# Kernel optimization log

Hardware: AMD Instinct MI355X
Metric: run time of the kernel (lower is better)

## Reference

```python
import jax, jax.numpy as jnp
import numpy as np

B, LQ, D, DFF, NH, DH, NL, NP = 8, 1024, 256, 1024, 8, 32, 3, 4
_SHAPES = np.array([[100, 100], [50, 50], [25, 25]], dtype=np.int32)  # (H, W) per level
_AREAS = _SHAPES[:, 0] * _SHAPES[:, 1]
LIN = int(_AREAS.sum())  # 13125
_STARTS = np.concatenate([[0], np.cumsum(_AREAS)[:-1]]).astype(np.int32)


def setup_inputs() -> dict:
    key = jax.random.key(0)
    ks = iter(jax.random.split(key, 64))
    def rn(shape, s=1.0):
        return jax.random.normal(next(ks), shape, jnp.float32) * s
    return {
        "query_embed": rn((B, LQ, D)),
        "query_mask": jnp.zeros((B, LQ), bool),  # True = padded key
        "query_order": rn((B, LQ, D)),
        "values": rn((B, LIN, D)),
        "ref_point": jax.random.uniform(next(ks), (B, LQ, 2), jnp.float32),
        "ref_pos": rn((B, LQ, D)),
        "ref_feat": rn((B, LQ, D)),
        "shapes": jnp.asarray(_SHAPES),
        "level_start": jnp.asarray(_STARTS),
        "headwise_refpoint_idxs": jnp.zeros((B, LQ), jnp.int32),  # unused (side_head=0)
        # self-attention sub-block params (nn.MultiheadAttention packed in-proj)
        "sa_in_w": rn((D, 3 * D), 0.02), "sa_in_b": jnp.zeros((3 * D,)),
        "sa_out_w": rn((D, D), 0.02), "sa_out_b": jnp.zeros((D,)),
        "sa_ln1_g": jnp.ones((D,)), "sa_ln1_b": jnp.zeros((D,)),
        "sa_l1_w": rn((D, DFF), 0.02), "sa_l1_b": jnp.zeros((DFF,)),
        "sa_l2_w": rn((DFF, D), 0.02), "sa_l2_b": jnp.zeros((D,)),
        "sa_ln2_g": jnp.ones((D,)), "sa_ln2_b": jnp.zeros((D,)),
        # MDeformAttn params
        "da_val_w": rn((D, D), 0.02), "da_val_b": jnp.zeros((D,)),
        "da_off_w": rn((D, NH * NL * NP * 2), 0.001), "da_off_b": rn((NH * NL * NP * 2,), 0.01),
        "da_att_w": rn((D, NH * NL * NP), 0.02), "da_att_b": jnp.zeros((NH * NL * NP,)),
        "da_out_w": rn((D, D), 0.02), "da_out_b": jnp.zeros((D,)),
        # post-deform FFN block params
        "ln1_g": jnp.ones((D,)), "ln1_b": jnp.zeros((D,)),
        "ff1_w": rn((D, DFF), 0.02), "ff1_b": jnp.zeros((DFF,)),
        "ff2_w": rn((DFF, D), 0.02), "ff2_b": jnp.zeros((D,)),
        "ln2_g": jnp.ones((D,)), "ln2_b": jnp.zeros((D,)),
    }


def _ln(x, g, b):
    m = jnp.mean(x, -1, keepdims=True)
    v = jnp.mean((x - m) ** 2, -1, keepdims=True)
    return (x - m) / jnp.sqrt(v + 1e-5) * g + b


def _mha(q, k, v, key_padding_mask, in_w, in_b, out_w, out_b):
    Bv = q.shape[0]
    qp = (q @ in_w[:, :D] + in_b[:D]).reshape(Bv, -1, NH, DH)
    kp = (k @ in_w[:, D:2 * D] + in_b[D:2 * D]).reshape(Bv, -1, NH, DH)
    vp = (v @ in_w[:, 2 * D:] + in_b[2 * D:]).reshape(Bv, -1, NH, DH)
    scores = jnp.einsum('bqhd,bkhd->bhqk', qp, kp) / jnp.sqrt(jnp.float32(DH))
    scores = scores + jnp.where(key_padding_mask[:, None, None, :], -1e9, 0.0)
    a = jax.nn.softmax(scores, -1)
    o = jnp.einsum('bhqk,bkhd->bqhd', a, vp).reshape(Bv, -1, D)
    return o @ out_w + out_b


def _ms_deform(query, ref_point, values, shapes,
               val_w, val_b, off_w, off_b, att_w, att_b, out_w, out_b):
    # Multi-scale deformable attention (MDeformAttn, align_corners=False bilinear, zero pad)
    Bv, Lq = query.shape[0], query.shape[1]
    v = (values @ val_w + val_b).reshape(Bv, -1, NH, DH)
    off = (query @ off_w + off_b).reshape(Bv, Lq, NH, NL, NP, 2)
    attn = jax.nn.softmax((query @ att_w + att_b).reshape(Bv, Lq, NH, NL * NP), -1)
    attn = attn.reshape(Bv, Lq, NH, NL, NP)
    norm = jnp.stack([shapes[:, 1], shapes[:, 0]], -1).astype(jnp.float32)  # (W, H)
    loc = ref_point[:, :, None, None, None, :] + off / norm[None, None, None, :, None, :]
    acc = 0.0
    for lvl in range(NL):  # static spatial shapes per level
        Hl, Wl = int(_SHAPES[lvl, 0]), int(_SHAPES[lvl, 1])
        s = int(_STARTS[lvl])
        vl = v[:, s:s + Hl * Wl].transpose(0, 2, 1, 3)  # [B,NH,Hl*Wl,DH]
        ll = loc[:, :, :, lvl]                          # [B,Lq,NH,NP,2]
        x = ll[..., 0] * Wl - 0.5
        y = ll[..., 1] * Hl - 0.5
        x0 = jnp.floor(x); y0 = jnp.floor(y)
        wx = x - x0; wy = y - y0
        x0i = x0.astype(jnp.int32); y0i = y0.astype(jnp.int32)
        def tw(w):  # [B,Lq,NH,NP] -> [B,NH,Lq*NP,1]
            return w.transpose(0, 2, 1, 3).reshape(Bv, NH, -1, 1)
        def gather(yy, xx):
            valid = ((yy >= 0) & (yy < Hl) & (xx >= 0) & (xx < Wl))
            idx = jnp.clip(yy, 0, Hl - 1) * Wl + jnp.clip(xx, 0, Wl - 1)
            idx_t = idx.transpose(0, 2, 1, 3).reshape(Bv, NH, -1)
            g = jnp.take_along_axis(vl, idx_t[..., None], axis=2)  # [B,NH,Lq*NP,DH]
            return g * tw(valid.astype(vl.dtype))
        samp = (tw((1 - wy) * (1 - wx)) * gather(y0i, x0i)
                + tw((1 - wy) * wx) * gather(y0i, x0i + 1)
                + tw(wy * (1 - wx)) * gather(y0i + 1, x0i)
                + tw(wy * wx) * gather(y0i + 1, x0i + 1))
        aw = tw(attn[:, :, :, lvl])
        acc = acc + (samp * aw).reshape(Bv, NH, Lq, NP, DH).sum(3)
    out = acc.transpose(0, 2, 1, 3).reshape(Bv, Lq, D)
    return out @ out_w + out_b


def reference(query_embed, query_mask, query_order, values, ref_point, ref_pos, ref_feat,
              shapes, level_start, headwise_refpoint_idxs,
              sa_in_w, sa_in_b, sa_out_w, sa_out_b, sa_ln1_g, sa_ln1_b,
              sa_l1_w, sa_l1_b, sa_l2_w, sa_l2_b, sa_ln2_g, sa_ln2_b,
              da_val_w, da_val_b, da_off_w, da_off_b, da_att_w, da_att_b, da_out_w, da_out_b,
              ln1_g, ln1_b, ff1_w, ff1_b, ff2_w, ff2_b, ln2_g, ln2_b):
    # forward_self_att(tgt + ref_feat, query_order + ref_pos, query_mask); dropout = identity (eval)
    src = query_embed + ref_feat
    pos = query_order + ref_pos
    q = src + pos
    src = _ln(src + _mha(q, q, src, query_mask, sa_in_w, sa_in_b, sa_out_w, sa_out_b), sa_ln1_g, sa_ln1_b)
    src = _ln(src + (jax.nn.relu(src @ sa_l1_w + sa_l1_b) @ sa_l2_w + sa_l2_b), sa_ln2_g, sa_ln2_b)
    tgt = src
    dq = tgt + query_order + ref_pos + ref_feat
    tgt2 = _ms_deform(dq, ref_point, values, shapes,
                      da_val_w, da_val_b, da_off_w, da_off_b, da_att_w, da_att_b, da_out_w, da_out_b)
    tgt = _ln(tgt + tgt2, ln1_g, ln1_b)
    tgt = _ln(tgt + (jax.nn.relu(tgt @ ff1_w + ff1_b) @ ff2_w + ff2_b), ln2_g, ln2_b)
    return tgt
```

## Files before the change

kernel.cpp:

```cpp
#include <hip/hip_runtime.h>
#include <math.h>

#define B_   8
#define LQ_  1024
#define D_   256
#define NH_  8
#define DH_  32
#define LIN_ 13125

typedef __attribute__((ext_vector_type(4))) float f32x4;
typedef __attribute__((ext_vector_type(8))) short bf16x8;
typedef __attribute__((ext_vector_type(4))) short bf16x4;

__device__ __forceinline__ float4 f4add(float4 a, float4 b){
  return make_float4(a.x+b.x, a.y+b.y, a.z+b.z, a.w+b.w);
}
__device__ __forceinline__ unsigned short f2bf(float f){
  unsigned u = __float_as_uint(f);
  unsigned r = (u + 0x7fffu + ((u>>16)&1u)) >> 16;
  return (unsigned short)r;
}
__device__ __forceinline__ float bf2f(unsigned short u){
  return __uint_as_float(((unsigned)u)<<16);
}
__device__ __forceinline__ unsigned pk2(float a, float b){
  return (unsigned)f2bf(a) | ((unsigned)f2bf(b)<<16);
}
__device__ __forceinline__ float fexp2(float x){
#if __has_builtin(__builtin_amdgcn_exp2f)
  return __builtin_amdgcn_exp2f(x);
#else
  return exp2f(x);
#endif
}
__device__ __forceinline__ f32x4 mfma16x16(bf16x4 a, bf16x4 b, f32x4 c){
#if __has_builtin(__builtin_amdgcn_mfma_f32_16x16x16_bf16)
  return __builtin_amdgcn_mfma_f32_16x16x16_bf16(a, b, c, 0, 0, 0);
#else
  asm volatile("s_nop 1\n\tv_mfma_f32_16x16x16_bf16 %0, %1, %2, %0"
               : "+v"(c) : "v"(a), "v"(b));
  return c;
#endif
}
__device__ __forceinline__ void gload16(const void* g, void* l){
  __builtin_amdgcn_global_load_lds(
      (const __attribute__((address_space(1))) void*)g,
      (__attribute__((address_space(3))) void*)l, 16, 0, 0);
}
__device__ __forceinline__ int xcd_swz(int lin, int nwg){
  if (nwg < 64) return lin;
  const int q = nwg >> 3, r = nwg & 7;
  const int x = lin & 7, d = lin >> 3;
  return (x < r ? x*(q+1) : r*(q+1) + (x-r)*q) + d;
}

__global__ __launch_bounds__(256) void k_prep(
    const float4* __restrict__ qe, const float4* __restrict__ rf,
    const float4* __restrict__ qo, const float4* __restrict__ rp,
    const unsigned char* __restrict__ mask,
    const float* __restrict__ off_b, const float* __restrict__ att_b,
    float4* __restrict__ src, uint2* __restrict__ srcb, uint2* __restrict__ qb,
    float* __restrict__ biasf, float* __restrict__ biasoa)
{
  int i = blockIdx.x*256 + threadIdx.x;
  if (i < B_*LQ_) biasf[i] = mask[i] ? -2.0e9f : 0.f;
  if (blockIdx.x == 32) {
    for (int j = threadIdx.x; j < 384; j += 256)
      biasoa[j] = (j < 192) ? off_b[j] : (j < 288 ? att_b[j-192] : 0.f);
  }
  float4 s = f4add(qe[i], rf[i]);
  src[i] = s;
  float4 q = f4add(s, f4add(qo[i], rp[i]));
  srcb[i] = make_uint2(pk2(s.x,s.y), pk2(s.z,s.w));
  qb[i]   = make_uint2(pk2(q.x,q.y), pk2(q.z,q.w));
}

struct WEnt { const float* s; unsigned short* d; int K; int N; };
struct WPack { WEnt e[10]; };
__global__ __launch_bounds__(256) void k_wtcvt(WPack p)
{
  __shared__ float sm[32][33];
  WEnt w = p.e[blockIdx.y];
  const int tk = w.K >> 5, tn = w.N >> 5;
  const int nt = tk * tn;
  const int r = threadIdx.x >> 5, c = threadIdx.x & 31;
  for (int tile = blockIdx.x; tile < nt; tile += gridDim.x) {
    const int ti = tile / tn, tj = tile % tn;
    #pragma unroll
    for (int rr = r; rr < 32; rr += 8)
      sm[rr][c] = w.s[(size_t)(ti*32+rr)*w.N + tj*32 + c];
    __syncthreads();
    #pragma unroll
    for (int rr = r; rr < 32; rr += 8)
      w.d[(size_t)(tj*32+rr)*w.K + ti*32 + c] = f2bf(sm[c][rr]);
    __syncthreads();
  }
}

__global__ __launch_bounds__(256) void k_f2b8(
    const float4* __restrict__ in, uint4* __restrict__ out)
{
  const int i = blockIdx.x*256 + threadIdx.x;
  float4 a = in[2*i], b = in[2*i+1];
  out[i] = make_uint4(pk2(a.x,a.y), pk2(a.z,a.w), pk2(b.x,b.y), pk2(b.z,b.w));
}

template<bool BF16OUT>
__global__ __launch_bounds__(256) void k_gemm_bf(
    const unsigned short* __restrict__ A, int lda,
    const unsigned short* __restrict__ Wt,
    const float* __restrict__ bias,
    float* __restrict__ Cf, unsigned short* __restrict__ Cb, int ldc,
    int M, int N, int K, int relu)
{
  __shared__ unsigned short As[2][4096];
  __shared__ unsigned short Bs[2][4096];
  const int t = threadIdx.x;
  const int lin = xcd_swz(blockIdx.y*gridDim.x + blockIdx.x, gridDim.x*gridDim.y);
  const int bx = lin % gridDim.x, by = lin / gridDim.x;
  const int m0 = by * 128;
  const int n0 = bx * 128;
  const int w  = t >> 6, lane = t & 63;
  const int lr = lane & 15, lg = lane >> 4;
  const int wm = (w & 1) * 64, wn = (w >> 1) * 64;

  const int rowc  = t >> 2;
  const int cbs8  = (((t & 3) ^ ((t >> 2) & 3)) << 3);
  const size_t ra0 = (size_t)min(m0 + rowc,      M-1) * lda;
  const size_t ra1 = (size_t)min(m0 + rowc + 64, M-1) * lda;
  const size_t rb0 = (size_t)(n0 + rowc)      * K;
  const size_t rb1 = (size_t)(n0 + rowc + 64) * K;
  unsigned short* la0[2] = { &As[0][(w<<9)],        &As[1][(w<<9)] };
  unsigned short* la1[2] = { &As[0][2048+(w<<9)],   &As[1][2048+(w<<9)] };
  unsigned short* lb0[2] = { &Bs[0][(w<<9)],        &Bs[1][(w<<9)] };
  unsigned short* lb1[2] = { &Bs[0][2048+(w<<9)],   &Bs[1][2048+(w<<9)] };

  f32x4 acc[4][4];
  #pragma unroll
  for (int i=0;i<4;++i)
    #pragma unroll
    for (int j=0;j<4;++j) acc[i][j] = (f32x4){0.f,0.f,0.f,0.f};

  const int cswz = ((lg ^ (lr & 3)) << 3);
  const int nt = K >> 5;

  {
    gload16(A  + ra0 + cbs8, la0[0]);
    gload16(A  + ra1 + cbs8, la1[0]);
    gload16(Wt + rb0 + cbs8, lb0[0]);
    gload16(Wt + rb1 + cbs8, lb1[0]);
  }
  for (int ks = 0; ks < nt; ++ks) {
    const int cur = ks & 1;
    __syncthreads();
    if (ks + 1 < nt) {
      const int kb = (ks + 1) << 5;
      const int nb = cur ^ 1;
      gload16(A  + ra0 + kb + cbs8, la0[nb]);
      gload16(A  + ra1 + kb + cbs8, la1[nb]);
      gload16(Wt + rb0 + kb + cbs8, lb0[nb]);
      gload16(Wt + rb1 + kb + cbs8, lb1[nb]);
    }
    bf16x8 af[4], bfr[4];
    #pragma unroll
    for (int mi=0;mi<4;++mi)
      af[mi]  = *reinterpret_cast<const bf16x8*>(&As[cur][(wm+mi*16+lr)*32 + cswz]);
    #pragma unroll
    for (int ni=0;ni<4;++ni)
      bfr[ni] = *reinterpret_cast<const bf16x8*>(&Bs[cur][(wn+ni*16+lr)*32 + cswz]);
    #pragma unroll
    for (int mi=0;mi<4;++mi)
      #pragma unroll
      for (int ni=0;ni<4;++ni)
        acc[mi][ni] = __builtin_amdgcn_mfma_f32_16x16x32_bf16(af[mi], bfr[ni], acc[mi][ni], 0, 0, 0);
  }

  float bs[4];
  #pragma unroll
  for (int ni=0;ni<4;++ni) bs[ni] = bias[n0 + wn + ni*16 + lr];
  #pragma unroll
  for (int mi=0;mi<4;++mi){
    #pragma unroll
    for (int i=0;i<4;++i){
      const int row = m0 + wm + mi*16 + lg*4 + i;
      if (row >= M) continue;
      #pragma unroll
      for (int ni=0;ni<4;++ni){
        const int col = n0 + wn + ni*16 + lr;
        float v = acc[mi][ni][i] + bs[ni];
        if (relu) v = fmaxf(v, 0.f);
        if (BF16OUT) Cb[(size_t)row*ldc + col] = f2bf(v);
        else         Cf[(size_t)row*ldc + col] = v;
      }
    }
  }
}

template<int EPI>
__global__ __launch_bounds__(256) void k_gemm64(
    const unsigned short* __restrict__ A, int lda,
    const unsigned short* __restrict__ Wt,
    const float* __restrict__ bias,
    float* __restrict__ Cf, unsigned short* __restrict__ Cb, int ldc,
    int M, int N, int K, int relu)
{
  __shared__ unsigned short As[2][4096];
  __shared__ unsigned short Bs[2][4096];
  const int t = threadIdx.x;
  const int lin = xcd_swz(blockIdx.y*gridDim.x + blockIdx.x, gridDim.x*gridDim.y);
  const int bx = lin % gridDim.x, by = lin / gridDim.x;
  const int m0 = by * 64;
  const int n0 = bx * 64;
  const int w = t >> 6, lane = t & 63;
  const int lr = lane & 15, lg = lane >> 4;
  const int wm = (w & 1) * 32, wn = (w >> 1) * 32;

  const int c0 = w*64 + lane;
  const int c1 = 256 + w*64 + lane;
  const int r0c = c0 >> 3, s0c = ((c0 & 7) ^ (r0c & 7)) << 3;
  const int r1c = c1 >> 3, s1c = ((c1 & 7) ^ (r1c & 7)) << 3;
  const size_t a0 = (size_t)(m0 + r0c)*lda + s0c;
  const size_t a1 = (size_t)(m0 + r1c)*lda + s1c;
  const size_t b0 = (size_t)(n0 + r0c)*K + s0c;
  const size_t b1 = (size_t)(n0 + r1c)*K + s1c;
  const int d0 = w*512, d1 = 2048 + w*512;

  f32x4 acc[2][2];
  acc[0][0]=acc[0][1]=acc[1][0]=acc[1][1]=(f32x4){0.f,0.f,0.f,0.f};

  gload16(A + a0, &As[0][d0]);  gload16(A + a1, &As[0][d1]);
  gload16(Wt + b0, &Bs[0][d0]); gload16(Wt + b1, &Bs[0][d1]);
  const int nt = K >> 6;
  for (int ks = 0; ks < nt; ++ks) {
    const int cur = ks & 1;
    __syncthreads();
    if (ks + 1 < nt) {
      const int kb = (ks + 1) << 6;
      const int nb = cur ^ 1;
      gload16(A + kb + a0, &As[nb][d0]);  gload16(A + kb + a1, &As[nb][d1]);
      gload16(Wt + kb + b0, &Bs[nb][d0]); gload16(Wt + kb + b1, &Bs[nb][d1]);
    }
    bf16x8 af[2][2], bfr[2][2];
    #pragma unroll
    for (int mi=0;mi<2;++mi){
      const int r = wm + mi*16 + lr;
      #pragma unroll
      for (int kk=0;kk<2;++kk){
        const int ch = ((kk*4 + lg) ^ (r & 7)) << 3;
        af[mi][kk] = *reinterpret_cast<const bf16x8*>(&As[cur][r*64 + ch]);
      }
    }
    #pragma unroll
    for (int ni=0;ni<2;++ni){
      const int r = wn + ni*16 + lr;
      #pragma unroll
      for (int kk=0;kk<2;++kk){
        const int ch = ((kk*4 + lg) ^ (r & 7)) << 3;
        bfr[ni][kk] = *reinterpret_cast<const bf16x8*>(&Bs[cur][r*64 + ch]);
      }
    }
    #pragma unroll
    for (int kk=0;kk<2;++kk)
      #pragma unroll
      for (int mi=0;mi<2;++mi)
        #pragma unroll
        for (int ni=0;ni<2;++ni)
          acc[mi][ni] = __builtin_amdgcn_mfma_f32_16x16x32_bf16(af[mi][kk], bfr[ni][kk], acc[mi][ni], 0, 0, 0);
  }

  float bs[2];
  bs[0] = bias[n0 + wn + lr];
  bs[1] = bias[n0 + wn + 16 + lr];
  if (EPI == 3) {
    #pragma unroll
    for (int mi=0;mi<2;++mi){
      const int rowb = m0 + wm + mi*16 + lg*4;
      #pragma unroll
      for (int ni=0;ni<2;++ni){
        const int colb = n0 + wn + ni*16 + lr;
        const int bh = (rowb >> 10)*8 + (colb >> 5);
        const int d = colb & 31;
        ushort4 pkv;
        pkv.x = f2bf(acc[mi][ni][0] + bs[ni]);
        pkv.y = f2bf(acc[mi][ni][1] + bs[ni]);
        pkv.z = f2bf(acc[mi][ni][2] + bs[ni]);
        pkv.w = f2bf(acc[mi][ni][3] + bs[ni]);
        *reinterpret_cast<ushort4*>(Cb + (size_t)bh*32768 + (size_t)d*1024 + (rowb & 1023)) = pkv;
      }
    }
    return;
  }
  #pragma unroll
  for (int mi=0;mi<2;++mi){
    #pragma unroll
    for (int i=0;i<4;++i){
      const int row = m0 + wm + mi*16 + lg*4 + i;
      #pragma unroll
      for (int ni=0;ni<2;++ni){
        const int col = n0 + wn + ni*16 + lr;
        float v = acc[mi][ni][i] + bs[ni];
        if (relu) v = fmaxf(v, 0.f);
        if (EPI == 0) {
          Cf[(size_t)row*ldc + col] = v;
        } else if (EPI == 1) {
          Cb[(size_t)row*ldc + col] = f2bf(v);
        } else {
          const int ch = col & 255;
          const int sel = col >> 8;
          const int bh = (row >> 10)*8 + (ch >> 5);
          Cb[(size_t)sel*2097152 + (size_t)bh*32768 + (size_t)(row & 1023)*32 + (ch & 31)] = f2bf(v);
        }
      }
    }
  }
}

__global__ __launch_bounds__(256) void k_gemm_ln(
    const unsigned short* __restrict__ A, int lda,
    const unsigned short* __restrict__ Wt,
    const float* __restrict__ bias,
    const float* __restrict__ X,
    const float* __restrict__ g, const float* __restrict__ be,
    float* __restrict__ out,
    unsigned short* __restrict__ ab,
    const float* __restrict__ qo, const float* __restrict__ rp,
    const float* __restrict__ rf, unsigned short* __restrict__ dqb,
    int K)
{
  __shared__ unsigned short As[2][1024];
  __shared__ unsigned short Bs[2][16384];
  __shared__ float part[4][16][2];
  const int t = threadIdx.x;
  const int w = t >> 6, lane = t & 63;
  const int lr = lane & 15, lg = lane >> 4;
  const int m0 = xcd_swz(blockIdx.x, gridDim.x) * 16;

  const int ar = t >> 3, ac = t & 7;
  const size_t aSrc = (size_t)(m0 + ar)*lda + ((ac ^ (ar & 7)) << 3);
  size_t bSrc[8];
  #pragma unroll
  for (int q=0;q<8;++q){
    const int c = q*256 + t;
    const int br = c >> 3, bc = c & 7;
    bSrc[q] = (size_t)br*K + ((bc ^ (br & 7)) << 3);
  }

  f32x4 acc[4];
  #pragma unroll
  for (int ni=0;ni<4;++ni) acc[ni] = (f32x4){0.f,0.f,0.f,0.f};

  if (w < 2) gload16(A + aSrc, &As[0][(w<<9)]);
  #pragma unroll
  for (int q=0;q<8;++q) gload16(Wt + bSrc[q], &Bs[0][q*2048 + (w<<9)]);

  const int nt = K >> 6;
  for (int ks = 0; ks < nt; ++ks) {
    const int cur = ks & 1;
    __syncthreads();
    if (ks + 1 < nt) {
      const int kb = (ks + 1) << 6;
      const int nb = cur ^ 1;
      if (w < 2) gload16(A + kb + aSrc, &As[nb][(w<<9)]);
      #pragma unroll
      for (int q=0;q<8;++q) gload16(Wt + kb + bSrc[q], &Bs[nb][q*2048 + (w<<9)]);
    }
    bf16x8 af[2];
    #pragma unroll
    for (int kk=0;kk<2;++kk){
      const int ch = ((kk*4 + lg) ^ (lr & 7)) << 3;
      af[kk] = *reinterpret_cast<const bf16x8*>(&As[cur][lr*64 + ch]);
    }
    #pragma unroll
    for (int ni=0;ni<4;++ni){
      const int r = w*64 + ni*16 + lr;
      #pragma unroll
      for (int kk=0;kk<2;++kk){
        const int ch = ((kk*4 + lg) ^ (r & 7)) << 3;
        bf16x8 bfv = *reinterpret_cast<const bf16x8*>(&Bs[cur][r*64 + ch]);
        acc[ni] = __builtin_amdgcn_mfma_f32_16x16x32_bf16(af[kk], bfv, acc[ni], 0, 0, 0);
      }
    }
  }

  float v[4][4];
  int colv[4];
  #pragma unroll
  for (int ni=0;ni<4;++ni) colv[ni] = w*64 + ni*16 + lr;
  #pragma unroll
  for (int ni=0;ni<4;++ni){
    const float bsv = bias[colv[ni]];
    #pragma unroll
    for (int i=0;i<4;++i){
      const int row = m0 + lg*4 + i;
      v[ni][i] = acc[ni][i] + bsv + X[(size_t)row*256 + colv[ni]];
    }
  }
  #pragma unroll
  for (int i=0;i<4;++i){
    float s1 = v[0][i]+v[1][i]+v[2][i]+v[3][i];
    float s2 = v[0][i]*v[0][i]+v[1][i]*v[1][i]+v[2][i]*v[2][i]+v[3][i]*v[3][i];
    #pragma unroll
    for (int o=1;o<16;o<<=1){ s1 += __shfl_xor(s1,o,64); s2 += __shfl_xor(s2,o,64); }
    if (lr == 0){ part[w][lg*4+i][0] = s1; part[w][lg*4+i][1] = s2; }
  }
  __syncthreads();
  #pragma unroll
  for (int i=0;i<4;++i){
    const int rl = lg*4 + i;
    const float S1 = part[0][rl][0]+part[1][rl][0]+part[2][rl][0]+part[3][rl][0];
    const float S2 = part[0][rl][1]+part[1][rl][1]+part[2][rl][1]+part[3][rl][1];
    const float mean = S1 * 0.00390625f;
    const float var  = S2 * 0.00390625f - mean*mean;
    const float rstd = rsqrtf(var + 1e-5f);
    const size_t row = m0 + rl;
    #pragma unroll
    for (int ni=0;ni<4;++ni){
      const int col = colv[ni];
      const float o = (v[ni][i]-mean)*rstd*g[col] + be[col];
      out[row*256 + col] = o;
      if (ab) ab[row*256 + col] = f2bf(o);
      if (dqb) {
        const float e = qo[row*256+col] + rp[row*256+col] + rf[row*256+col];
        dqb[row*256 + col] = f2bf(o + e);
      }
    }
  }
}

__global__ __launch_bounds__(256) void k_attn2(
    const unsigned short* __restrict__ Qbf,
    const unsigned short* __restrict__ Kbf,
    const unsigned short* __restrict__ Vtb,
    const float* __restrict__ biasf,
    unsigned short* __restrict__ Ob)
{
  __shared__ unsigned short Klds[2][2048];
  __shared__ unsigned short Vlds[2][2048];
  __shared__ float Blds[1024];
  const int t = threadIdx.x;
  const int wv = t >> 6, lane = t & 63;
  const int lin = xcd_swz(blockIdx.y*gridDim.x + blockIdx.x, gridDim.x*gridDim.y);
  const int bx = lin % gridDim.x, by = lin / gridDim.x;
  const int qt = bx * 4 + wv;
  const int bh = by;
  const int b = bh >> 3;
  const int q0 = qt << 4;
  const int lr = lane & 15, lg = lane >> 4;

  bf16x8 qf = *reinterpret_cast<const bf16x8*>(
      Qbf + (size_t)bh*32768 + (size_t)(q0 + lr)*32 + lg*8);

  *reinterpret_cast<float4*>(&Blds[t*4]) =
      *reinterpret_cast<const float4*>(biasf + b*1024 + t*4);

  const unsigned short* Kg = Kbf + (size_t)bh*32768;
  const unsigned short* Vg = Vtb + (size_t)bh*32768;

  const int kRow   = lane >> 2;
  const int kChunk = (lane & 3) ^ (kRow & 3);
  const size_t kSrc = (size_t)(wv*16 + kRow)*32 + (kChunk<<3);
  const int vDim   = lane >> 3;
  const int vChunk = (lane & 7) ^ vDim;
  const size_t vSrc = (size_t)(wv*8 + vDim)*1024 + (vChunk<<3);
  unsigned short* kDst[2] = { &Klds[0][wv<<9], &Klds[1][wv<<9] };
  unsigned short* vDst[2] = { &Vlds[0][wv<<9], &Vlds[1][wv<<9] };

  gload16(Kg + kSrc, kDst[0]);
  gload16(Vg + vSrc, vDst[0]);
  __syncthreads();

  f32x4 acc0 = {0.f,0.f,0.f,0.f}, acc1 = {0.f,0.f,0.f,0.f};
  float m_run = -1e30f, l_run = 0.f;
  const float Cs = 0.17677669529663687f * 1.4426950408889634f;
  const int kswz = (lg ^ (lr & 3)) << 3;

  for (int kt = 0; kt < 16; ++kt) {
    const int cur = kt & 1;
    if (kt + 1 < 16) {
      const size_t k0n = (size_t)(kt + 1) << 6;
      gload16(Kg + k0n*32 + kSrc, kDst[cur^1]);
      gload16(Vg + k0n    + vSrc, vDst[cur^1]);
    }
    f32x4 st[4];
    __builtin_amdgcn_s_setprio(1);
    #pragma unroll
    for (int j=0;j<4;++j){
      bf16x8 kf = *reinterpret_cast<const bf16x8*>(&Klds[cur][(16*j + lr)*32 + kswz]);
      f32x4 z = {0.f,0.f,0.f,0.f};
      st[j] = __builtin_amdgcn_mfma_f32_16x16x32_bf16(kf, qf, z, 0, 0, 0);
    }
    __builtin_amdgcn_s_setprio(0);
    const int k0 = kt << 6;
    float s[16];
    #pragma unroll
    for (int j=0;j<4;++j){
      float4 bv = *reinterpret_cast<const float4*>(&Blds[k0 + 16*j + lg*4]);
      s[4*j+0] = fmaf(st[j][0], Cs, bv.x);
      s[4*j+1] = fmaf(st[j][1], Cs, bv.y);
      s[4*j+2] = fmaf(st[j][2], Cs, bv.z);
      s[4*j+3] = fmaf(st[j][3], Cs, bv.w);
    }
    float mc = fmaxf(fmaxf(fmaxf(s[0],s[1]),fmaxf(s[2],s[3])),
                     fmaxf(fmaxf(s[4],s[5]),fmaxf(s[6],s[7])));
    float mc2 = fmaxf(fmaxf(fmaxf(s[8],s[9]),fmaxf(s[10],s[11])),
                      fmaxf(fmaxf(s[12],s[13]),fmaxf(s[14],s[15])));
    mc = fmaxf(mc, mc2);
    mc = fmaxf(mc, __shfl_xor(mc, 16, 64));
    mc = fmaxf(mc, __shfl_xor(mc, 32, 64));
    if (!__all(mc <= m_run + 8.f)) {
      float m_new = fmaxf(m_run, mc);
      float sc = fexp2(m_run - m_new);
      l_run *= sc;
      m_run = m_new;
      float sc0 = __shfl(sc, lg*4+0, 64);
      float sc1 = __shfl(sc, lg*4+1, 64);
      float sc2 = __shfl(sc, lg*4+2, 64);
      float sc3 = __shfl(sc, lg*4+3, 64);
      acc0[0]*=sc0; acc0[1]*=sc1; acc0[2]*=sc2; acc0[3]*=sc3;
      acc1[0]*=sc0; acc1[1]*=sc1; acc1[2]*=sc2; acc1[3]*=sc3;
    }
    float p[16];
    #pragma unroll
    for (int i=0;i<16;++i) p[i] = fexp2(s[i] - m_run);
    float ps = 0.f;
    #pragma unroll
    for (int i=0;i<16;++i) ps += p[i];
    ps += __shfl_xor(ps, 16, 64);
    ps += __shfl_xor(ps, 32, 64);
    l_run += ps;
    bf16x4 pb[4];
    #pragma unroll
    for (int j=0;j<4;++j){
      unsigned lo, hi;
      asm("v_cvt_pk_bf16_f32 %0, %1, %2" : "=v"(lo) : "v"(p[4*j+0]), "v"(p[4*j+1]));
      asm("v_cvt_pk_bf16_f32 %0, %1, %2" : "=v"(hi) : "v"(p[4*j+2]), "v"(p[4*j+3]));
      uint2 u = make_uint2(lo, hi);
      pb[j] = __builtin_bit_cast(bf16x4, u);
    }
    __builtin_amdgcn_s_setprio(1);
    #pragma unroll
    for (int j=0;j<4;++j){
      const int coff = (((2*j + (lg>>1)) ^ (lr & 7)) << 3) + ((lg & 1) << 2);
      bf16x4 v0 = *reinterpret_cast<const bf16x4*>(&Vlds[cur][lr*64 + coff]);
      bf16x4 v1 = *reinterpret_cast<const bf16x4*>(&Vlds[cur][(16+lr)*64 + coff]);
      acc0 = mfma16x16(pb[j], v0, acc0);
      acc1 = mfma16x16(pb[j], v1, acc1);
    }
    __builtin_amdgcn_s_setprio(0);
    __syncthreads();
  }
  float li[4];
  #pragma unroll
  for (int i=0;i<4;++i) li[i] = 1.f / __shfl(l_run, lg*4+i, 64);
  const int h = bh & 7;
  unsigned short* orow = Ob + (size_t)(b*1024 + q0)*256 + h*32;
  #pragma unroll
  for (int i=0;i<4;++i){
    orow[(size_t)(lg*4+i)*256 + lr]      = f2bf(acc0[i]*li[i]);
    orow[(size_t)(lg*4+i)*256 + 16 + lr] = f2bf(acc1[i]*li[i]);
  }
}

__global__ __launch_bounds__(256) void k_dgather2(
    const unsigned short* __restrict__ vproj,
    const float* __restrict__ IJ,
    const float* __restrict__ refp,
    unsigned short* __restrict__ outb)
{
  __shared__ int   ilds[8][12][4];
  __shared__ float wlds[8][12][4];
  const int t = threadIdx.x;
  const int bq = blockIdx.x;
  const int h = t >> 5;
  const int p = t & 31;
  if (p < 12) {
    const float* al = IJ + (size_t)bq*384 + 192 + h*12;
    float lg[12];
    float mx = -INFINITY;
    #pragma unroll
    for (int i=0;i<12;++i){ lg[i] = al[i]; mx = fmaxf(mx, lg[i]); }
    float se = 0.f;
    #pragma unroll
    for (int i=0;i<12;++i) se += __expf(lg[i]-mx);
    const float aw = __expf(lg[p]-mx) / se;
    const float rx = refp[(size_t)bq*2+0], ry = refp[(size_t)bq*2+1];
    const float ox = IJ[(size_t)bq*384 + h*24 + 2*p];
    const float oy = IJ[(size_t)bq*384 + h*24 + 2*p + 1];
    const int l = p >> 2;
    const int WW[3]={100,50,25}, SS[3]={0,10000,12500};
    const int Wi = WW[l], Hi = WW[l], s0 = SS[l];
    const float Wf = (float)Wi, Hf = (float)Hi;
    const float x = (rx + ox/Wf)*Wf - 0.5f;
    const float y = (ry + oy/Hf)*Hf - 0.5f;
    const float x0f = floorf(x), y0f = floorf(y);
    const float wx = x - x0f, wy = y - y0f;
    const int x0 = (int)x0f, y0 = (int)y0f;
    const int xs0 = min(max(x0,0),Wi-1),   xs1 = min(max(x0+1,0),Wi-1);
    const int ys0 = min(max(y0,0),Hi-1),   ys1 = min(max(y0+1,0),Hi-1);
    const bool vx0 = (x0>=0)&&(x0<Wi),     vx1 = (x0+1>=0)&&(x0+1<Wi);
    const bool vy0 = (y0>=0)&&(y0<Hi),     vy1 = (y0+1>=0)&&(y0+1<Hi);
    const int vb = (bq >> 10) * LIN_;
    ilds[h][p][0] = vb + s0 + ys0*Wi + xs0;
    ilds[h][p][1] = vb + s0 + ys0*Wi + xs1;
    ilds[h][p][2] = vb + s0 + ys1*Wi + xs0;
    ilds[h][p][3] = vb + s0 + ys1*Wi + xs1;
    wlds[h][p][0] = (vy0&&vx0)? (1.f-wy)*(1.f-wx)*aw : 0.f;
    wlds[h][p][1] = (vy0&&vx1)? (1.f-wy)*wx*aw       : 0.f;
    wlds[h][p][2] = (vy1&&vx0)? wy*(1.f-wx)*aw       : 0.f;
    wlds[h][p][3] = (vy1&&vx1)? wy*wx*aw             : 0.f;
  }
  __syncthreads();
  const int col = t;
  float acc = 0.f;
  #pragma unroll
  for (int pt=0; pt<12; ++pt){
    acc = fmaf(wlds[h][pt][0], bf2f(vproj[(size_t)ilds[h][pt][0]*256 + col]), acc);
    acc = fmaf(wlds[h][pt][1], bf2f(vproj[(size_t)ilds[h][pt][1]*256 + col]), acc);
    acc = fmaf(wlds[h][pt][2], bf2f(vproj[(size_t)ilds[h][pt][2]*256 + col]), acc);
    acc = fmaf(wlds[h][pt][3], bf2f(vproj[(size_t)ilds[h][pt][3]*256 + col]), acc);
  }
  outb[(size_t)bq*256 + col] = f2bf(acc);
}

extern "C" void kernel_launch(void* const* d_in, const int* in_sizes, int n_in,
                              void* d_out, int out_size, void* d_ws, size_t ws_size,
                              hipStream_t stream)
{
  const float* qe      = (const float*)d_in[0];
  const unsigned char* qmask = (const unsigned char*)d_in[1];
  const float* qo      = (const float*)d_in[2];
  const float* values  = (const float*)d_in[3];
  const float* refp    = (const float*)d_in[4];
  const float* rp      = (const float*)d_in[5];
  const float* rf      = (const float*)d_in[6];
  const float* sa_in_w = (const float*)d_in[10];
  const float* sa_in_b = (const float*)d_in[11];
  const float* sa_out_w= (const float*)d_in[12];
  const float* sa_out_b= (const float*)d_in[13];
  const float* sa_ln1_g= (const float*)d_in[14];
  const float* sa_ln1_b= (const float*)d_in[15];
  const float* sa_l1_w = (const float*)d_in[16];
  const float* sa_l1_b = (const float*)d_in[17];
  const float* sa_l2_w = (const float*)d_in[18];
  const float* sa_l2_b = (const float*)d_in[19];
  const float* sa_ln2_g= (const float*)d_in[20];
  const float* sa_ln2_b= (const float*)d_in[21];
  const float* da_val_w= (const float*)d_in[22];
  const float* da_val_b= (const float*)d_in[23];
  const float* da_off_w= (const float*)d_in[24];
  const float* da_off_b= (const float*)d_in[25];
  const float* da_att_w= (const float*)d_in[26];
  const float* da_att_b= (const float*)d_in[27];
  const float* da_out_w= (const float*)d_in[28];
  const float* da_out_b= (const float*)d_in[29];
  const float* ln1_g   = (const float*)d_in[30];
  const float* ln1_b   = (const float*)d_in[31];
  const float* ff1_w   = (const float*)d_in[32];
  const float* ff1_b   = (const float*)d_in[33];
  const float* ff2_w   = (const float*)d_in[34];
  const float* ff2_b   = (const float*)d_in[35];
  const float* ln2_g   = (const float*)d_in[36];
  const float* ln2_b   = (const float*)d_in[37];

  float* Wk = (float*)d_ws;
  const size_t MEG = 1u<<20;
  float* A   = Wk;
  unsigned short* Ab   = (unsigned short*)(Wk + 4*MEG);
  unsigned short* hidb = (unsigned short*)(Wk + 5*MEG);
  unsigned short* WT   = (unsigned short*)(Wk + 9*MEG);
  unsigned short* qb   = (unsigned short*)(Wk + 10*MEG);
  unsigned short* srcb = (unsigned short*)(Wk + 11*MEG);
  unsigned short* Qbf  = (unsigned short*)(Wk + 12*MEG);
  unsigned short* Kbf  = (unsigned short*)(Wk + 13*MEG);
  unsigned short* Vtb  = (unsigned short*)(Wk + 15*MEG);
  unsigned short* aob  = (unsigned short*)(Wk + 16*MEG);
  unsigned short* dqb  = (unsigned short*)(Wk + 10*MEG);
  float* IJ = Wk + 12*MEG;
  unsigned short* vb = (unsigned short*)(Wk + 23*MEG);
  unsigned short* Hb = (unsigned short*)(Wk + 37*MEG);
  unsigned short* dG = (unsigned short*)(Wk + 51*MEG);
  float* biasf  = Wk + 52*MEG;
  float* biasoa = Wk + 52*MEG + 8192;

  unsigned short* sa_inT  = WT;
  unsigned short* sa_outT = WT + 196608;
  unsigned short* sa_l1T  = WT + 262144;
  unsigned short* sa_l2T  = WT + 524288;
  unsigned short* da_valT = WT + 786432;
  unsigned short* da_outT = WT + 851968;
  unsigned short* ff1T    = WT + 917504;
  unsigned short* ff2T    = WT + 1179648;
  unsigned short* offattT = WT + 1441792;

  WPack wp_;
  wp_.e[0] = { sa_in_w, sa_inT, 256, 768 };
  wp_.e[1] = { sa_out_w, sa_outT, 256, 256 };
  wp_.e[2] = { sa_l1_w, sa_l1T, 256, 1024 };
  wp_.e[3] = { sa_l2_w, sa_l2T, 1024, 256 };
  wp_.e[4] = { da_val_w, da_valT, 256, 256 };
  wp_.e[5] = { da_out_w, da_outT, 256, 256 };
  wp_.e[6] = { ff1_w, ff1T, 256, 1024 };
  wp_.e[7] = { ff2_w, ff2T, 1024, 256 };
  wp_.e[8] = { da_off_w, offattT, 256, 192 };
  wp_.e[9] = { da_att_w, offattT + 192*256, 256, 96 };

  dim3 blk(256);
  k_wtcvt<<<dim3(64,10), blk, 0, stream>>>(wp_);
  k_f2b8<<<13125, blk, 0, stream>>>((const float4*)values, (uint4*)vb);
  k_prep<<<2048, blk, 0, stream>>>((const float4*)qe,(const float4*)rf,
                                   (const float4*)qo,(const float4*)rp,
                                   qmask, da_off_b, da_att_b,
                                   (float4*)A,(uint2*)srcb,(uint2*)qb,
                                   biasf, biasoa);
  k_gemm64<2><<<dim3(8,128), blk, 0, stream>>>(qb,256, sa_inT, sa_in_b, nullptr,Qbf,0, 8192,512,256, 0);
  k_gemm64<3><<<dim3(4,128), blk, 0, stream>>>(srcb,256, sa_inT+512*256, sa_in_b+512, nullptr,Vtb,0, 8192,256,256, 0);
  k_attn2<<<dim3(16,64), blk, 0, stream>>>(Qbf, Kbf, Vtb, biasf, aob);
  k_gemm_ln<<<512, blk, 0, stream>>>(aob,256, sa_outT, sa_out_b, A,
                                     sa_ln1_g, sa_ln1_b, A, Ab,
                                     nullptr, nullptr, nullptr, nullptr, 256);
  k_gemm_bf<true><<<dim3(8,64), blk, 0, stream>>>(Ab,256, sa_l1T, sa_l1_b, nullptr,hidb,1024, 8192,1024,256, 1);
  k_gemm_ln<<<512, blk, 0, stream>>>(hidb,1024, sa_l2T, sa_l2_b, A,
                                     sa_ln2_g, sa_ln2_b, A, Ab,
                                     qo, rp, rf, dqb, 1024);
  k_gemm64<0><<<dim3(6,128), blk, 0, stream>>>(dqb,256, offattT, biasoa, IJ,nullptr,384, 8192,384,256, 0);
  k_gemm_bf<true><<<dim3(2,821), blk, 0, stream>>>(vb,256, da_valT, da_val_b, nullptr,Hb,256, 105000,256,256, 0);
  k_dgather2<<<8192, blk, 0, stream>>>(Hb, IJ, refp, dG);
  k_gemm_ln<<<512, blk, 0, stream>>>(dG,256, da_outT, da_out_b, A,
                                     ln1_g, ln1_b, A, Ab,
                                     nullptr, nullptr, nullptr, nullptr, 256);
  k_gemm_bf<true><<<dim3(8,64), blk, 0, stream>>>(Ab,256, ff1T, ff1_b, nullptr,hidb,1024, 8192,1024,256, 1);
  k_gemm_ln<<<512, blk, 0, stream>>>(hidb,1024, ff2T, ff2_b, A,
                                     ln2_g, ln2_b, (float*)d_out, nullptr,
                                     nullptr, nullptr, nullptr, nullptr, 1024);
}
```

Measured before the change: 243.7 us.

## Fuse fp32-to-bf16 conversion of values into the value-projection GEMM

Removes the standalone kernel that converted the 105000x256 fp32 values tensor to bf16, and adds a dedicated value-projection GEMM. The new GEMM reads fp32 rows directly, converts them in registers with packed bf16 conversion instructions, and keeps the whole 128x256 weight slice resident in swizzled LDS. Each block covers 256 rows with register double-buffering of A loads and uses 16x16x32 MFMA. This drops one full write and re-read of the bf16 copy, but the GEMM now loads fp32 from global memory without staging it through LDS, and it uses more registers.

New measurement: 235.7 us. -3.3%, faster.

```diff
diff --git a/kernel.cpp b/kernel.cpp
--- a/kernel.cpp
+++ b/kernel.cpp
@@ -46,6 +46,15 @@
   __builtin_amdgcn_global_load_lds(
       (const __attribute__((address_space(1))) void*)g,
       (__attribute__((address_space(3))) void*)l, 16, 0, 0);
+}
+__device__ __forceinline__ bf16x8 cvt8(const float4& a, const float4& b){
+  unsigned u0,u1,u2,u3;
+  asm("v_cvt_pk_bf16_f32 %0, %1, %2" : "=v"(u0) : "v"(a.x), "v"(a.y));
+  asm("v_cvt_pk_bf16_f32 %0, %1, %2" : "=v"(u1) : "v"(a.z), "v"(a.w));
+  asm("v_cvt_pk_bf16_f32 %0, %1, %2" : "=v"(u2) : "v"(b.x), "v"(b.y));
+  asm("v_cvt_pk_bf16_f32 %0, %1, %2" : "=v"(u3) : "v"(b.z), "v"(b.w));
+  uint4 uu = make_uint4(u0,u1,u2,u3);
+  return __builtin_bit_cast(bf16x8, uu);
 }
 __device__ __forceinline__ int xcd_swz(int lin, int nwg){
   if (nwg < 64) return lin;
@@ -95,14 +104,6 @@
       w.d[(size_t)(tj*32+rr)*w.K + ti*32 + c] = f2bf(sm[c][rr]);
     __syncthreads();
   }
-}
-
-__global__ __launch_bounds__(256) void k_f2b8(
-    const float4* __restrict__ in, uint4* __restrict__ out)
-{
-  const int i = blockIdx.x*256 + threadIdx.x;
-  float4 a = in[2*i], b = in[2*i+1];
-  out[i] = make_uint4(pk2(a.x,a.y), pk2(a.z,a.w), pk2(b.x,b.y), pk2(b.z,b.w));
 }
 
 template<bool BF16OUT>
@@ -191,6 +192,87 @@
         if (relu) v = fmaxf(v, 0.f);
         if (BF16OUT) Cb[(size_t)row*ldc + col] = f2bf(v);
         else         Cf[(size_t)row*ldc + col] = v;
+      }
+    }
+  }
+}
+
+__global__ __launch_bounds__(256, 2) void k_gemm_vp(
+    const float* __restrict__ A,
+    const unsigned short* __restrict__ Wt,
+    const float* __restrict__ bias,
+    unsigned short* __restrict__ Cb, int M)
+{
+  __shared__ unsigned short Ws[32768];
+  const int t = threadIdx.x;
+  const int lin = xcd_swz(blockIdx.y*gridDim.x + blockIdx.x, gridDim.x*gridDim.y);
+  const int bx = lin % gridDim.x, by = lin / gridDim.x;
+  const int n0 = bx * 128;
+  const int m0 = by * 256;
+  const int w = t >> 6, lane = t & 63;
+  const int lr = lane & 15, lg = lane >> 4;
+
+  #pragma unroll
+  for (int q = 0; q < 16; ++q) {
+    const int c = q*256 + t;
+    const int row = c >> 5, pos = c & 31;
+    gload16(Wt + (size_t)(n0 + row)*256 + ((pos ^ (row & 31)) << 3),
+            (unsigned short*)Ws + (size_t)c*8);
+  }
+  __syncthreads();
+
+  float bs[8];
+  #pragma unroll
+  for (int ni=0;ni<8;++ni) bs[ni] = bias[n0 + ni*16 + lr];
+
+  const int mw = m0 + w*64;
+  float4 avA[8][2], avB[8][2];
+  #pragma unroll
+  for (int kk=0;kk<8;++kk){
+    const size_t ad = (size_t)min(mw + lr, M-1)*256 + kk*32 + lg*8;
+    avA[kk][0] = *reinterpret_cast<const float4*>(A + ad);
+    avA[kk][1] = *reinterpret_cast<const float4*>(A + ad + 4);
+  }
+  #pragma unroll
+  for (int s = 0; s < 4; ++s) {
+    const int mb = mw + s*16;
+    if (s < 3) {
+      #pragma unroll
+      for (int kk=0;kk<8;++kk){
+        const size_t ad = (size_t)min(mb + 16 + lr, M-1)*256 + kk*32 + lg*8;
+        if (s & 1) {
+          avA[kk][0] = *reinterpret_cast<const float4*>(A + ad);
+          avA[kk][1] = *reinterpret_cast<const float4*>(A + ad + 4);
+        } else {
+          avB[kk][0] = *reinterpret_cast<const float4*>(A + ad);
+          avB[kk][1] = *reinterpret_cast<const float4*>(A + ad + 4);
+        }
+      }
+    }
+    bf16x8 af[8];
+    #pragma unroll
+    for (int kk=0;kk<8;++kk)
+      af[kk] = (s & 1) ? cvt8(avB[kk][0], avB[kk][1]) : cvt8(avA[kk][0], avA[kk][1]);
+    f32x4 acc[8];
+    #pragma unroll
+    for (int ni=0;ni<8;++ni) acc[ni] = (f32x4){0.f,0.f,0.f,0.f};
+    #pragma unroll
+    for (int kk=0;kk<8;++kk){
+      #pragma unroll
+      for (int ni=0;ni<8;++ni){
+        const int r = ni*16 + lr;
+        const int p = (kk*4 + lg) ^ (r & 31);
+        bf16x8 wf = *reinterpret_cast<const bf16x8*>(&Ws[r*256 + (p<<3)]);
+        acc[ni] = __builtin_amdgcn_mfma_f32_16x16x32_bf16(af[kk], wf, acc[ni], 0, 0, 0);
+      }
+    }
+    #pragma unroll
+    for (int ni=0;ni<8;++ni){
+      const int col = n0 + ni*16 + lr;
+      #pragma unroll
+      for (int i=0;i<4;++i){
+        const int row = mb + lg*4 + i;
+        if (row < M) Cb[(size_t)row*256 + col] = f2bf(acc[ni][i] + bs[ni]);
       }
     }
   }
@@ -676,7 +758,6 @@
   unsigned short* aob  = (unsigned short*)(Wk + 16*MEG);
   unsigned short* dqb  = (unsigned short*)(Wk + 10*MEG);
   float* IJ = Wk + 12*MEG;
-  unsigned short* vb = (unsigned short*)(Wk + 23*MEG);
   unsigned short* Hb = (unsigned short*)(Wk + 37*MEG);
   unsigned short* dG = (unsigned short*)(Wk + 51*MEG);
   float* biasf  = Wk + 52*MEG;
@@ -706,7 +787,6 @@
 
   dim3 blk(256);
   k_wtcvt<<<dim3(64,10), blk, 0, stream>>>(wp_);
-  k_f2b8<<<13125, blk, 0, stream>>>((const float4*)values, (uint4*)vb);
   k_prep<<<2048, blk, 0, stream>>>((const float4*)qe,(const float4*)rf,
                                    (const float4*)qo,(const float4*)rp,
                                    qmask, da_off_b, da_att_b,
@@ -723,7 +803,7 @@
                                      sa_ln2_g, sa_ln2_b, A, Ab,
                                      qo, rp, rf, dqb, 1024);
   k_gemm64<0><<<dim3(6,128), blk, 0, stream>>>(dqb,256, offattT, biasoa, IJ,nullptr,384, 8192,384,256, 0);
-  k_gemm_bf<true><<<dim3(2,821), blk, 0, stream>>>(vb,256, da_valT, da_val_b, nullptr,Hb,256, 105000,256,256, 0);
+  k_gemm_vp<<<dim3(2,411), blk, 0, stream>>>(values, da_valT, da_val_b, Hb, 105000);
   k_dgather2<<<8192, blk, 0, stream>>>(Hb, IJ, refp, dG);
   k_gemm_ln<<<512, blk, 0, stream>>>(dG,256, da_outT, da_out_b, A,
                                      ln1_g, ln1_b, A, Ab,
```
